# Performance work log

Hardware: AMD Instinct MI355X
Metric: run time of the kernel (lower is better)

The kernel has to match this reference:

```python
import jax, jax.numpy as jnp
import numpy as np

DIM = 1024
NUM_HEADS = 16
HEAD_DIM = DIM // NUM_HEADS
SCALE = HEAD_DIM ** -0.5


def setup_inputs() -> dict:
    key = jax.random.key(0)
    ks = jax.random.split(key, 5)
    x = jax.random.normal(ks[0], (4, 1024, DIM), dtype=jnp.float32)
    w_qkv = jax.random.normal(ks[1], (DIM, 3 * DIM), dtype=jnp.float32) * (DIM ** -0.5)
    b_qkv = jnp.zeros((3 * DIM,), dtype=jnp.float32)
    w_proj = jax.random.normal(ks[2], (DIM, DIM), dtype=jnp.float32) * (DIM ** -0.5)
    b_proj = jnp.zeros((DIM,), dtype=jnp.float32)
    return {"x": x, "w_qkv": w_qkv, "b_qkv": b_qkv, "w_proj": w_proj, "b_proj": b_proj}


def reference(x, w_qkv, b_qkv, w_proj, b_proj):
    B, N, C = x.shape
    qkv = x @ w_qkv + b_qkv                                  # [B, N, 3C]
    qkv = qkv.reshape(B, N, 3, NUM_HEADS, HEAD_DIM)
    qkv = jnp.transpose(qkv, (2, 0, 3, 1, 4))                # [3, B, H, N, d]
    q, k, v = qkv[0] * SCALE, qkv[1], qkv[2]
    # attn scores in float32 (clamp to finfo range is a no-op after the cast)
    attn = jnp.einsum('bhnd,bhmd->bhnm', q, k).astype(jnp.float32)
    f32 = jnp.finfo(jnp.float32)
    attn = jnp.clip(attn, f32.min, f32.max)
    attn = jax.nn.softmax(attn, axis=-1)
    out = jnp.einsum('bhnm,bhmd->bhnd', attn, v)             # [B, H, N, d]
    out = jnp.transpose(out, (0, 2, 1, 3)).reshape(B, N, C)
    return out @ w_proj + b_proj
```

## Files before the change

### kernel.cpp

```cpp
#include <hip/hip_runtime.h>


typedef _Float16 half8 __attribute__((ext_vector_type(8)));
typedef _Float16 half4v __attribute__((ext_vector_type(4)));
typedef __fp16 fp16x2 __attribute__((ext_vector_type(2)));
typedef float floatx4 __attribute__((ext_vector_type(4)));

#define MFMA16(a, b, c) __builtin_amdgcn_mfma_f32_16x16x32_f16((a), (b), (c), 0, 0, 0)

static constexpr int DIM = 1024;
static constexpr int BATCH = 4;
static constexpr int SEQ = 1024;
static constexpr int NH = 16;
static constexpr int HD = 64;
static constexpr float SCALE = 0.125f;

__device__ static inline void gld16(_Float16* lds, const _Float16* g) {
    __builtin_amdgcn_global_load_lds(
        (const __attribute__((address_space(1))) void*)g,
        (__attribute__((address_space(3))) void*)lds, 16, 0, 0);
}

__global__ __launch_bounds__(256) void prep(const float* __restrict__ x,
                                            _Float16* __restrict__ xh,
                                            const float* __restrict__ wqkv,
                                            _Float16* __restrict__ wqkvT,
                                            const float* __restrict__ wproj,
                                            _Float16* __restrict__ wprojT) {
    __shared__ float tile[32][33];
    const int bid = blockIdx.x;
    const int tid = threadIdx.x;
    if (bid < 4096) {
        int i = (bid * 256 + tid) * 4;
        float4 v = *reinterpret_cast<const float4*>(x + i);
        half4v h;
        h[0] = (_Float16)v.x; h[1] = (_Float16)v.y;
        h[2] = (_Float16)v.z; h[3] = (_Float16)v.w;
        const int m = i >> 10, k = i & 1023;
        *reinterpret_cast<half4v*>(
            &xh[((size_t)(k >> 5) * 4096 + m) * 32 + (k & 31)]) = h;
        return;
    }
    const float* in;
    _Float16* out;
    int C, NN, bx, by;
    if (bid < 7168) {
        int b = bid - 4096;
        in = wqkv; out = wqkvT; C = 3072; NN = 3072;
        bx = b % 96; by = b / 96;
    } else {
        int b = bid - 7168;
        in = wproj; out = wprojT; C = 1024; NN = 1024;
        bx = b & 31; by = b >> 5;
    }
    const int c0 = bx * 32, r0 = by * 32;
    const int tx = tid & 31, ty = tid >> 5;
#pragma unroll
    for (int j = 0; j < 32; j += 8)
        tile[ty + j][tx] = in[(size_t)(r0 + ty + j) * C + (c0 + tx)];
    __syncthreads();
#pragma unroll
    for (int j = 0; j < 32; j += 8)
        out[((size_t)(r0 >> 5) * NN + (c0 + ty + j)) * 32 + tx] =
            (_Float16)tile[tx][ty + j];
}

template <int MODE>
__global__ __launch_bounds__(256) void gemm_bt(const _Float16* __restrict__ A,
                                               const _Float16* __restrict__ Bt,
                                               const float* __restrict__ bias, int N,
                                               float* __restrict__ outF,
                                               _Float16* __restrict__ qbuf,
                                               _Float16* __restrict__ kbuf,
                                               _Float16* __restrict__ vtbuf) {
    constexpr int NT = 32;
    __shared__ _Float16 S[4][2][4096];

    const int tid = threadIdx.x;
    const int wid = tid >> 6;
    const int lane = tid & 63;
    const int g = lane >> 4;
    const int ln = lane & 15;
    const int wr = wid >> 1, wc = wid & 1;
    const int m0 = blockIdx.y * 128;
    const int n0 = blockIdx.x * 128;
    const size_t PA = (size_t)4096 * 32;
    const size_t PB = (size_t)N * 32;
    const int lsw = (lane >> 2) * 32 + (((lane & 3) ^ ((lane >> 3) & 3)) * 8);
    const int gsw = (g ^ ((ln >> 1) & 3)) * 8;
    const _Float16* ga = A + ((size_t)(m0 + wr * 64)) * 32 + lsw;
    const _Float16* gb = Bt + ((size_t)(n0 + wc * 64)) * 32 + lsw;
    _Float16* Sw = &S[wid][0][0];

    floatx4 acc[4][4];
#pragma unroll
    for (int i = 0; i < 4; ++i)
#pragma unroll
        for (int j = 0; j < 4; ++j) acc[i][j] = (floatx4){0.f, 0.f, 0.f, 0.f};

#pragma unroll
    for (int c = 0; c < 4; ++c) {
        gld16(Sw + c * 512, ga + c * 512);
        gld16(Sw + 2048 + c * 512, gb + c * 512);
    }

    for (int kt = 0; kt < NT; ++kt) {
        const int cur = kt & 1;
        if (kt < NT - 1) {
            const size_t ka = (size_t)(kt + 1) * PA;
            const size_t kb = (size_t)(kt + 1) * PB;
            _Float16* Sn = Sw + (cur ^ 1) * 4096;
#pragma unroll
            for (int c = 0; c < 4; ++c) {
                gld16(Sn + c * 512, ga + ka + c * 512);
                gld16(Sn + 2048 + c * 512, gb + kb + c * 512);
            }
            asm volatile("s_waitcnt vmcnt(8)" ::: "memory");
        } else {
            asm volatile("s_waitcnt vmcnt(0)" ::: "memory");
        }
        const _Float16* Sc = Sw + cur * 4096;

        half8 af[4], bf[4];
#pragma unroll
        for (int i = 0; i < 4; ++i)
            af[i] = *reinterpret_cast<const half8*>(&Sc[(i * 16 + ln) * 32 + gsw]);
#pragma unroll
        for (int j = 0; j < 4; ++j)
            bf[j] = *reinterpret_cast<const half8*>(&Sc[2048 + (j * 16 + ln) * 32 + gsw]);
#pragma unroll
        for (int i = 0; i < 4; ++i)
#pragma unroll
            for (int j = 0; j < 4; ++j) acc[i][j] = MFMA16(af[i], bf[j], acc[i][j]);
    }

#pragma unroll
    for (int i = 0; i < 4; ++i) {
#pragma unroll
        for (int j = 0; j < 4; ++j) {
            const int n = n0 + wc * 64 + j * 16 + ln;
            const float bn = bias[n];
            const int mrow = m0 + wr * 64 + i * 16 + g * 4;
            if (MODE == 0) {
                const int which = n >> 10;
                const int rem = n & 1023;
                const int h = rem >> 6;
                const int dd = rem & 63;
                const int b = mrow >> 10, tok = mrow & 1023;
                const int bh = b * NH + h;
                if (which == 2) {
                    half4v pk;
#pragma unroll
                    for (int r = 0; r < 4; ++r) pk[r] = (_Float16)(acc[i][j][r] + bn);
                    *reinterpret_cast<half4v*>(
                        &vtbuf[((size_t)(bh * 32 + (tok >> 5)) * 64 + dd) * 32 +
                               (tok & 31)]) = pk;
                } else if (which == 1) {
#pragma unroll
                    for (int r = 0; r < 4; ++r)
                        kbuf[((size_t)(bh * 2 + (dd >> 5)) * SEQ + tok + r) * 32 +
                             (dd & 31)] = (_Float16)(acc[i][j][r] + bn);
                } else {
#pragma unroll
                    for (int r = 0; r < 4; ++r)
                        qbuf[(size_t)((bh << 10) + tok + r) * HD + dd] =
                            (_Float16)((acc[i][j][r] + bn) * SCALE);
                }
            } else {
#pragma unroll
                for (int r = 0; r < 4; ++r)
                    outF[(size_t)(mrow + r) * N + n] = acc[i][j][r] + bn;
            }
        }
    }
}

__global__ __launch_bounds__(256, 4) void flash_attn(const _Float16* __restrict__ qbuf,
                                                     const _Float16* __restrict__ kbuf,
                                                     const _Float16* __restrict__ vtbuf,
                                                     _Float16* __restrict__ attn_out) {
    __shared__ _Float16 Klds[2 * 4096];
    __shared__ _Float16 Vlds[2 * 4096];

    const int tid = threadIdx.x;
    const int wid = tid >> 6;
    const int lane = tid & 63;
    const int g = lane >> 4;
    const int ln = lane & 15;
    const int bh = blockIdx.x;
    const int qbase = blockIdx.y * 64 + wid * 16;
    const _Float16* qg = qbuf + ((size_t)bh << 10) * HD;
    const _Float16* kg = kbuf + (size_t)bh * (2 * SEQ * 32);
    const _Float16* vg = vtbuf + (size_t)bh * (32 * 64 * 32);

    const int woff = wid * 512;
    const int lsw = (lane >> 2) * 32 + (((lane & 3) ^ ((lane >> 3) & 3)) * 8);
    const int gsw = (g ^ ((ln >> 1) & 3)) * 8;
    const int sl0 = ((lane >> 4) & 1) * 32 + ln;
    const bool hi32 = (lane & 32) != 0;

    half8 qf[2];
#pragma unroll
    for (int f = 0; f < 2; ++f)
        qf[f] = *reinterpret_cast<const half8*>(
            qg + (size_t)(qbase + ln) * HD + f * 32 + g * 8);

    floatx4 o[4];
#pragma unroll
    for (int t = 0; t < 4; ++t) o[t] = (floatx4){0.f, 0.f, 0.f, 0.f};
    float l_lane = 0.f;

    constexpr int NT = SEQ / 64;
#pragma unroll
    for (int f = 0; f < 2; ++f) {
        gld16(&Klds[f * 2048 + woff], kg + (size_t)f * (SEQ * 32) + woff + lsw);
        gld16(&Vlds[f * 2048 + woff], vg + (size_t)f * 2048 + woff + lsw);
    }

    for (int kt = 0; kt < NT; ++kt) {
        asm volatile("s_waitcnt vmcnt(0)" ::: "memory");
        asm volatile("s_barrier" ::: "memory");
        const int cur = kt & 1;
        if (kt < NT - 1) {
            const int nb = cur ^ 1;
#pragma unroll
            for (int f = 0; f < 2; ++f) {
                gld16(&Klds[nb * 4096 + f * 2048 + woff],
                      kg + (size_t)f * (SEQ * 32) + (kt + 1) * 2048 + woff + lsw);
                gld16(&Vlds[nb * 4096 + f * 2048 + woff],
                      vg + (size_t)(2 * (kt + 1) + f) * 2048 + woff + lsw);
            }
        }
        const _Float16* Kb = &Klds[cur * 4096];
        const _Float16* Vb = &Vlds[cur * 4096];

        half8 kf[4][2], vf[4][2];
#pragma unroll
        for (int c = 0; c < 4; ++c)
#pragma unroll
            for (int f = 0; f < 2; ++f) {
                kf[c][f] = *reinterpret_cast<const half8*>(
                    &Kb[f * 2048 + (c * 16 + ln) * 32 + gsw]);
                vf[c][f] = *reinterpret_cast<const half8*>(
                    &Vb[f * 2048 + (c * 16 + ln) * 32 + gsw]);
            }

        floatx4 st[4];
#pragma unroll
        for (int c = 0; c < 4; ++c) {
            floatx4 z = (floatx4){0.f, 0.f, 0.f, 0.f};
            z = MFMA16(kf[c][0], qf[0], z);
            z = MFMA16(kf[c][1], qf[1], z);
            st[c] = z;
        }

        int pk[4][2];
#pragma unroll
        for (int c = 0; c < 4; ++c) {
            float p0 = __expf(st[c][0]);
            float p1 = __expf(st[c][1]);
            float p2 = __expf(st[c][2]);
            float p3 = __expf(st[c][3]);
            l_lane += (p0 + p1) + (p2 + p3);
            union { fp16x2 h; int i; } u0, u1;
            u0.h = __builtin_amdgcn_cvt_pkrtz(p0, p1);
            u1.h = __builtin_amdgcn_cvt_pkrtz(p2, p3);
            pk[c][0] = u0.i;
            pk[c][1] = u1.i;
        }

#pragma unroll
        for (int H = 0; H < 2; ++H) {
            int a0 = __shfl(pk[2 * H][0], sl0), b0 = __shfl(pk[2 * H + 1][0], sl0);
            int a1 = __shfl(pk[2 * H][1], sl0), b1 = __shfl(pk[2 * H + 1][1], sl0);
            int a2 = __shfl(pk[2 * H][0], sl0 + 16), b2 = __shfl(pk[2 * H + 1][0], sl0 + 16);
            int a3 = __shfl(pk[2 * H][1], sl0 + 16), b3 = __shfl(pk[2 * H + 1][1], sl0 + 16);
            union { int i[4]; half8 h; } ua;
            ua.i[0] = hi32 ? b0 : a0;
            ua.i[1] = hi32 ? b1 : a1;
            ua.i[2] = hi32 ? b2 : a2;
            ua.i[3] = hi32 ? b3 : a3;
#pragma unroll
            for (int t = 0; t < 4; ++t) o[t] = MFMA16(ua.h, vf[t][H], o[t]);
        }
    }

    l_lane += __shfl_xor(l_lane, 16);
    l_lane += __shfl_xor(l_lane, 32);

    const int b = bh >> 4, h = bh & 15;
#pragma unroll
    for (int r = 0; r < 4; ++r) {
        const float inv = 1.0f / __shfl(l_lane, g * 4 + r);
        const int tok = qbase + g * 4 + r;
#pragma unroll
        for (int t = 0; t < 4; ++t)
            attn_out[((size_t)(h * 2 + (t >> 1)) * 4096 + (b * SEQ + tok)) * 32 +
                     (t & 1) * 16 + ln] = (_Float16)(o[t][r] * inv);
    }
}

extern "C" void kernel_launch(void* const* d_in, const int* in_sizes, int n_in,
                              void* d_out, int out_size, void* d_ws, size_t ws_size,
                              hipStream_t stream) {
    const float* x = (const float*)d_in[0];
    const float* wqkv = (const float*)d_in[1];
    const float* bqkv = (const float*)d_in[2];
    const float* wproj = (const float*)d_in[3];
    const float* bproj = (const float*)d_in[4];
    float* out = (float*)d_out;

    char* ws = (char*)d_ws;
    _Float16* xh     = (_Float16*)(ws);
    _Float16* wqkvT  = (_Float16*)(ws + (8ull << 20));
    _Float16* qbuf   = (_Float16*)(ws + (14ull << 20));
    _Float16* kbuf   = (_Float16*)(ws + (22ull << 20));
    _Float16* vtbuf  = (_Float16*)(ws + (30ull << 20));
    _Float16* wprojT = (_Float16*)(ws + (38ull << 20));
    _Float16* attn   = xh;

    prep<<<8192, 256, 0, stream>>>(x, xh, wqkv, wqkvT, wproj, wprojT);
    gemm_bt<0><<<dim3(24, 32), 256, 0, stream>>>(xh, wqkvT, bqkv, 3 * DIM, nullptr,
                                                 qbuf, kbuf, vtbuf);
    flash_attn<<<dim3(BATCH * NH, SEQ / 64), 256, 0, stream>>>(qbuf, kbuf, vtbuf, attn);
    gemm_bt<1><<<dim3(8, 32), 256, 0, stream>>>(attn, wprojT, bproj, DIM, out,
                                                nullptr, nullptr, nullptr);
}
```

Measured before the change: 177.3 us.

## Use 256x256-tile 512-thread GEMM with 4-stage LDS pipeline for QKV projection

Adds a new gemm256 kernel with 256x256 output tiles, 8 waves, and a 4-buffer global_load_lds pipeline that issues next-stage loads interleaved with MFMA halves, and uses it for the QKV projection instead of the 128x128 gemm_bt. Larger tiles raise arithmetic intensity and cut global/L2 traffic per FLOP, and the deeper prefetch hides load latency. The grid shrinks to 192 blocks, fewer than the number of CUs on the device, so per-CU occupancy and load balance may suffer. Register pressure from 32 accumulators per wave is also a risk.

```diff
diff --git a/kernel.cpp b/kernel.cpp
--- a/kernel.cpp
+++ b/kernel.cpp
@@ -66,6 +66,135 @@
 }
 
 template <int MODE>
+__global__ __launch_bounds__(512, 2) void gemm256(const _Float16* __restrict__ A,
+                                                  const _Float16* __restrict__ Bt,
+                                                  const float* __restrict__ bias,
+                                                  int N, float* __restrict__ outF,
+                                                  _Float16* __restrict__ qbuf,
+                                                  _Float16* __restrict__ kbuf,
+                                                  _Float16* __restrict__ vtbuf) {
+    __shared__ __align__(16) _Float16 S[4][16384];
+
+    const int tid = threadIdx.x;
+    const int wid = tid >> 6;
+    const int lane = tid & 63;
+    const int g = lane >> 4;
+    const int ln = lane & 15;
+    const int wr = wid >> 2, wc = wid & 3;
+    const int m0 = blockIdx.y * 256;
+    const int n0 = blockIdx.x * 256;
+    const size_t PA = (size_t)4096 * 32;
+    const size_t PB = (size_t)N * 32;
+    const int lsw = (lane >> 2) * 32 + (((lane & 3) ^ ((lane >> 3) & 3)) * 8);
+    const int gsw = (g ^ ((ln >> 1) & 3)) * 8;
+    const _Float16* ga = A + ((size_t)(m0 + wid * 32)) * 32 + lsw;
+    const _Float16* gb = Bt + ((size_t)(n0 + wid * 32)) * 32 + lsw;
+
+    floatx4 acc[8][4];
+#pragma unroll
+    for (int i = 0; i < 8; ++i)
+#pragma unroll
+        for (int j = 0; j < 4; ++j) acc[i][j] = (floatx4){0.f, 0.f, 0.f, 0.f};
+
+#define STAGE_A(t)                                                      \
+    do {                                                                \
+        const _Float16* s_ = ga + (size_t)(t) * PA;                     \
+        _Float16* d_ = &S[(t) & 3][wid * 1024];                         \
+        gld16(d_, s_);                                                  \
+        gld16(d_ + 512, s_ + 512);                                      \
+    } while (0)
+#define STAGE_B(t)                                                      \
+    do {                                                                \
+        const _Float16* s_ = gb + (size_t)(t) * PB;                     \
+        _Float16* d_ = &S[(t) & 3][8192 + wid * 1024];                  \
+        gld16(d_, s_);                                                  \
+        gld16(d_ + 512, s_ + 512);                                      \
+    } while (0)
+
+    STAGE_A(0); STAGE_B(0);
+    STAGE_A(1); STAGE_B(1);
+    STAGE_A(2); STAGE_B(2);
+
+#define COMPUTE_HALF(Sc, rh)                                                     \
+    do {                                                                         \
+        half8 af[4];                                                             \
+        _Pragma("unroll") for (int i = 0; i < 4; ++i) af[i] =                    \
+            *reinterpret_cast<const half8*>(                                     \
+                &(Sc)[(wr * 128 + (rh) * 64 + i * 16 + ln) * 32 + gsw]);         \
+        __builtin_amdgcn_s_setprio(1);                                           \
+        _Pragma("unroll") for (int i = 0; i < 4; ++i)                            \
+            _Pragma("unroll") for (int j = 0; j < 4; ++j) acc[(rh) * 4 + i][j] = \
+                MFMA16(af[i], bf[j], acc[(rh) * 4 + i][j]);                      \
+        __builtin_amdgcn_s_setprio(0);                                           \
+    } while (0)
+
+#define GEMM_STEP(t, DO_STAGE, GATE_N)                                          \
+    do {                                                                        \
+        asm volatile("s_waitcnt vmcnt(" GATE_N ")" ::: "memory");               \
+        __builtin_amdgcn_s_barrier();                                           \
+        const _Float16* Sc = &S[(t) & 3][0];                                    \
+        if (DO_STAGE) STAGE_A((t) + 3);                                         \
+        half8 bf[4];                                                            \
+        _Pragma("unroll") for (int j = 0; j < 4; ++j) bf[j] =                   \
+            *reinterpret_cast<const half8*>(                                    \
+                &Sc[8192 + (wc * 64 + j * 16 + ln) * 32 + gsw]);                \
+        COMPUTE_HALF(Sc, 0);                                                    \
+        if (DO_STAGE) STAGE_B((t) + 3);                                        \
+        COMPUTE_HALF(Sc, 1);                                                    \
+    } while (0)
+
+    for (int t = 0; t < 29; ++t) GEMM_STEP(t, true, "8");
+    GEMM_STEP(29, false, "8");
+    GEMM_STEP(30, false, "4");
+    GEMM_STEP(31, false, "0");
+
+#undef GEMM_STEP
+#undef COMPUTE_HALF
+#undef STAGE_A
+#undef STAGE_B
+
+#pragma unroll
+    for (int i = 0; i < 8; ++i) {
+#pragma unroll
+        for (int j = 0; j < 4; ++j) {
+            const int n = n0 + wc * 64 + j * 16 + ln;
+            const float bn = bias[n];
+            const int mrow = m0 + wr * 128 + i * 16 + g * 4;
+            if (MODE == 0) {
+                const int which = n >> 10;
+                const int rem = n & 1023;
+                const int h = rem >> 6;
+                const int dd = rem & 63;
+                const int b = mrow >> 10, tok = mrow & 1023;
+                const int bh = b * NH + h;
+                if (which == 2) {
+                    half4v pk;
+#pragma unroll
+                    for (int r = 0; r < 4; ++r) pk[r] = (_Float16)(acc[i][j][r] + bn);
+                    *reinterpret_cast<half4v*>(
+                        &vtbuf[((size_t)(bh * 32 + (tok >> 5)) * 64 + dd) * 32 +
+                               (tok & 31)]) = pk;
+                } else if (which == 1) {
+#pragma unroll
+                    for (int r = 0; r < 4; ++r)
+                        kbuf[((size_t)(bh * 2 + (dd >> 5)) * SEQ + tok + r) * 32 +
+                             (dd & 31)] = (_Float16)(acc[i][j][r] + bn);
+                } else {
+#pragma unroll
+                    for (int r = 0; r < 4; ++r)
+                        qbuf[(size_t)((bh << 10) + tok + r) * HD + dd] =
+                            (_Float16)((acc[i][j][r] + bn) * SCALE);
+                }
+            } else {
+#pragma unroll
+                for (int r = 0; r < 4; ++r)
+                    outF[(size_t)(mrow + r) * N + n] = acc[i][j][r] + bn;
+            }
+        }
+    }
+}
+
+template <int MODE>
 __global__ __launch_bounds__(256) void gemm_bt(const _Float16* __restrict__ A,
                                                const _Float16* __restrict__ Bt,
                                                const float* __restrict__ bias, int N,
@@ -320,7 +449,7 @@
     _Float16* attn   = xh;
 
     prep<<<8192, 256, 0, stream>>>(x, xh, wqkv, wqkvT, wproj, wprojT);
-    gemm_bt<0><<<dim3(24, 32), 256, 0, stream>>>(xh, wqkvT, bqkv, 3 * DIM, nullptr,
+    gemm256<0><<<dim3(12, 16), 512, 0, stream>>>(xh, wqkvT, bqkv, 3 * DIM, nullptr,
                                                  qbuf, kbuf, vtbuf);
     flash_attn<<<dim3(BATCH * NH, SEQ / 64), 256, 0, stream>>>(qbuf, kbuf, vtbuf, attn);
     gemm_bt<1><<<dim3(8, 32), 256, 0, stream>>>(attn, wprojT, bproj, DIM, out,
```

Result: faster. 170.4 us (-3.9%).

## Rewrite GEMMs with shared LDS tiles, 4-stage pipeline and larger QKV tiles

Applied to the files above, without the earlier changes.

Replaces the templated per-wave GEMM, where each wave loaded its own private A/B tiles, with two specialised kernels of 512 threads. All eight waves now share one block-wide LDS tile, and a 4-deep global_load_lds ring uses barriers, staggered waitcnts and s_setprio around the MFMA bursts. The QKV GEMM moves to 256x192 tiles (a 16x16 grid) to raise data reuse per block. The change aims to cut redundant global/LDS traffic and hide load latency. In exchange it adds barrier synchronisation, uses more LDS per block, and launches fewer blocks, which may underfill the CUs.

```diff
diff --git a/kernel.cpp b/kernel.cpp
--- a/kernel.cpp
+++ b/kernel.cpp
@@ -65,16 +65,134 @@
             (_Float16)tile[tx][ty + j];
 }
 
-template <int MODE>
-__global__ __launch_bounds__(256) void gemm_bt(const _Float16* __restrict__ A,
-                                               const _Float16* __restrict__ Bt,
-                                               const float* __restrict__ bias, int N,
-                                               float* __restrict__ outF,
-                                               _Float16* __restrict__ qbuf,
-                                               _Float16* __restrict__ kbuf,
-                                               _Float16* __restrict__ vtbuf) {
-    constexpr int NT = 32;
-    __shared__ _Float16 S[4][2][4096];
+__global__ __launch_bounds__(512, 2) void gemm_qkv(const _Float16* __restrict__ A,
+                                                   const _Float16* __restrict__ Bt,
+                                                   const float* __restrict__ bias,
+                                                   _Float16* __restrict__ qbuf,
+                                                   _Float16* __restrict__ kbuf,
+                                                   _Float16* __restrict__ vtbuf) {
+    __shared__ __align__(16) _Float16 S[4][14336];
+
+    const int tid = threadIdx.x;
+    const int wid = tid >> 6;
+    const int lane = tid & 63;
+    const int g = lane >> 4;
+    const int ln = lane & 15;
+    const int wr = wid >> 1, wc = wid & 1;
+    const int m0 = blockIdx.y * 256;
+    const int n0 = blockIdx.x * 192;
+    const bool wlt4 = wid < 4;
+    const size_t PA = (size_t)4096 * 32;
+    const size_t PB = (size_t)3072 * 32;
+    const int lsw = (lane >> 2) * 32 + (((lane & 3) ^ ((lane >> 3) & 3)) * 8);
+    const int gsw = (g ^ ((ln >> 1) & 3)) * 8;
+    const _Float16* ga0 = A + (size_t)(m0 + wid * 16) * 32 + lsw;
+    const _Float16* ga1 = A + (size_t)(m0 + (wid + 8) * 16) * 32 + lsw;
+    const _Float16* gb0 = Bt + (size_t)(n0 + wid * 16) * 32 + lsw;
+    const _Float16* gb1 = Bt + (size_t)(n0 + (wid + 8) * 16) * 32 + lsw;
+
+    floatx4 acc[4][6];
+#pragma unroll
+    for (int i = 0; i < 4; ++i)
+#pragma unroll
+        for (int j = 0; j < 6; ++j) acc[i][j] = (floatx4){0.f, 0.f, 0.f, 0.f};
+
+#define STAGE_A(t)                                                      \
+    do {                                                                \
+        gld16(&S[(t) & 3][wid * 512], ga0 + (size_t)(t) * PA);          \
+        gld16(&S[(t) & 3][(wid + 8) * 512], ga1 + (size_t)(t) * PA);    \
+    } while (0)
+#define STAGE_B(t)                                                      \
+    do {                                                                \
+        gld16(&S[(t) & 3][8192 + wid * 512], gb0 + (size_t)(t) * PB);   \
+        if (wlt4)                                                       \
+            gld16(&S[(t) & 3][8192 + (wid + 8) * 512],                  \
+                  gb1 + (size_t)(t) * PB);                              \
+    } while (0)
+
+    STAGE_A(0); STAGE_B(0);
+    STAGE_A(1); STAGE_B(1);
+    STAGE_A(2); STAGE_B(2);
+
+#define COMPUTE_HALF(Sc, hh)                                                   \
+    do {                                                                       \
+        half8 af[2];                                                           \
+        _Pragma("unroll") for (int i = 0; i < 2; ++i) af[i] =                  \
+            *reinterpret_cast<const half8*>(                                   \
+                &(Sc)[(wr * 64 + (hh) * 32 + i * 16 + ln) * 32 + gsw]);        \
+        __builtin_amdgcn_s_setprio(1);                                         \
+        _Pragma("unroll") for (int i = 0; i < 2; ++i)                          \
+            _Pragma("unroll") for (int j = 0; j < 6; ++j)                      \
+                acc[(hh) * 2 + i][j] = MFMA16(af[i], bf[j], acc[(hh) * 2 + i][j]); \
+        __builtin_amdgcn_s_setprio(0);                                         \
+    } while (0)
+
+#define QKV_STEP(t, DO_STAGE, G4, G3)                                          \
+    do {                                                                       \
+        if (wlt4) asm volatile("s_waitcnt vmcnt(" G4 ")" ::: "memory");        \
+        else      asm volatile("s_waitcnt vmcnt(" G3 ")" ::: "memory");        \
+        __builtin_amdgcn_s_barrier();                                          \
+        const _Float16* Sc = &S[(t) & 3][0];                                   \
+        if (DO_STAGE) STAGE_A((t) + 3);                                        \
+        half8 bf[6];                                                           \
+        _Pragma("unroll") for (int j = 0; j < 6; ++j) bf[j] =                  \
+            *reinterpret_cast<const half8*>(                                   \
+                &Sc[8192 + (wc * 96 + j * 16 + ln) * 32 + gsw]);               \
+        COMPUTE_HALF(Sc, 0);                                                   \
+        if (DO_STAGE) STAGE_B((t) + 3);                                        \
+        COMPUTE_HALF(Sc, 1);                                                   \
+    } while (0)
+
+    for (int t = 0; t < 29; ++t) QKV_STEP(t, true, "8", "6");
+    QKV_STEP(29, false, "8", "6");
+    QKV_STEP(30, false, "4", "3");
+    QKV_STEP(31, false, "0", "0");
+
+#undef QKV_STEP
+#undef COMPUTE_HALF
+#undef STAGE_A
+#undef STAGE_B
+
+#pragma unroll
+    for (int i = 0; i < 4; ++i) {
+#pragma unroll
+        for (int j = 0; j < 6; ++j) {
+            const int n = n0 + wc * 96 + j * 16 + ln;
+            const float bn = bias[n];
+            const int mrow = m0 + wr * 64 + i * 16 + g * 4;
+            const int which = n >> 10;
+            const int rem = n & 1023;
+            const int h = rem >> 6;
+            const int dd = rem & 63;
+            const int b = mrow >> 10, tok = mrow & 1023;
+            const int bh = b * NH + h;
+            if (which == 2) {
+                half4v pk;
+#pragma unroll
+                for (int r = 0; r < 4; ++r) pk[r] = (_Float16)(acc[i][j][r] + bn);
+                *reinterpret_cast<half4v*>(
+                    &vtbuf[((size_t)(bh * 32 + (tok >> 5)) * 64 + dd) * 32 +
+                           (tok & 31)]) = pk;
+            } else if (which == 1) {
+#pragma unroll
+                for (int r = 0; r < 4; ++r)
+                    kbuf[((size_t)(bh * 2 + (dd >> 5)) * SEQ + tok + r) * 32 +
+                         (dd & 31)] = (_Float16)(acc[i][j][r] + bn);
+            } else {
+#pragma unroll
+                for (int r = 0; r < 4; ++r)
+                    qbuf[(size_t)((bh << 10) + tok + r) * HD + dd] =
+                        (_Float16)((acc[i][j][r] + bn) * SCALE);
+            }
+        }
+    }
+}
+
+__global__ __launch_bounds__(512, 2) void gemm_proj(const _Float16* __restrict__ A,
+                                                    const _Float16* __restrict__ Bt,
+                                                    const float* __restrict__ bias,
+                                                    float* __restrict__ outF) {
+    __shared__ __align__(16) _Float16 S[4][8192];
 
     const int tid = threadIdx.x;
     const int wid = tid >> 6;
@@ -85,92 +203,70 @@
     const int m0 = blockIdx.y * 128;
     const int n0 = blockIdx.x * 128;
     const size_t PA = (size_t)4096 * 32;
-    const size_t PB = (size_t)N * 32;
+    const size_t PB = (size_t)1024 * 32;
     const int lsw = (lane >> 2) * 32 + (((lane & 3) ^ ((lane >> 3) & 3)) * 8);
     const int gsw = (g ^ ((ln >> 1) & 3)) * 8;
-    const _Float16* ga = A + ((size_t)(m0 + wr * 64)) * 32 + lsw;
-    const _Float16* gb = Bt + ((size_t)(n0 + wc * 64)) * 32 + lsw;
-    _Float16* Sw = &S[wid][0][0];
-
-    floatx4 acc[4][4];
-#pragma unroll
-    for (int i = 0; i < 4; ++i)
+    const _Float16* ga = A + (size_t)(m0 + wid * 16) * 32 + lsw;
+    const _Float16* gb = Bt + (size_t)(n0 + wid * 16) * 32 + lsw;
+
+    floatx4 acc[2][4];
+#pragma unroll
+    for (int i = 0; i < 2; ++i)
 #pragma unroll
         for (int j = 0; j < 4; ++j) acc[i][j] = (floatx4){0.f, 0.f, 0.f, 0.f};
 
-#pragma unroll
-    for (int c = 0; c < 4; ++c) {
-        gld16(Sw + c * 512, ga + c * 512);
-        gld16(Sw + 2048 + c * 512, gb + c * 512);
-    }
-
-    for (int kt = 0; kt < NT; ++kt) {
-        const int cur = kt & 1;
-        if (kt < NT - 1) {
-            const size_t ka = (size_t)(kt + 1) * PA;
-            const size_t kb = (size_t)(kt + 1) * PB;
-            _Float16* Sn = Sw + (cur ^ 1) * 4096;
-#pragma unroll
-            for (int c = 0; c < 4; ++c) {
-                gld16(Sn + c * 512, ga + ka + c * 512);
-                gld16(Sn + 2048 + c * 512, gb + kb + c * 512);
-            }
-            asm volatile("s_waitcnt vmcnt(8)" ::: "memory");
-        } else {
-            asm volatile("s_waitcnt vmcnt(0)" ::: "memory");
-        }
-        const _Float16* Sc = Sw + cur * 4096;
-
-        half8 af[4], bf[4];
-#pragma unroll
-        for (int i = 0; i < 4; ++i)
-            af[i] = *reinterpret_cast<const half8*>(&Sc[(i * 16 + ln) * 32 + gsw]);
-#pragma unroll
-        for (int j = 0; j < 4; ++j)
-            bf[j] = *reinterpret_cast<const half8*>(&Sc[2048 + (j * 16 + ln) * 32 + gsw]);
-#pragma unroll
-        for (int i = 0; i < 4; ++i)
-#pragma unroll
-            for (int j = 0; j < 4; ++j) acc[i][j] = MFMA16(af[i], bf[j], acc[i][j]);
-    }
-
-#pragma unroll
-    for (int i = 0; i < 4; ++i) {
+#define STAGE_A(t) gld16(&S[(t) & 3][wid * 512], ga + (size_t)(t) * PA)
+#define STAGE_B(t) gld16(&S[(t) & 3][4096 + wid * 512], gb + (size_t)(t) * PB)
+
+    STAGE_A(0); STAGE_B(0);
+    STAGE_A(1); STAGE_B(1);
+    STAGE_A(2); STAGE_B(2);
+
+#define COMPUTE_HALF(Sc, hh)                                                   \
+    do {                                                                       \
+        half8 af = *reinterpret_cast<const half8*>(                            \
+            &(Sc)[(wr * 32 + (hh) * 16 + ln) * 32 + gsw]);                     \
+        __builtin_amdgcn_s_setprio(1);                                         \
+        _Pragma("unroll") for (int j = 0; j < 4; ++j)                          \
+            acc[hh][j] = MFMA16(af, bf[j], acc[hh][j]);                        \
+        __builtin_amdgcn_s_setprio(0);                                         \
+    } while (0)
+
+#define PROJ_STEP(t, DO_STAGE, GN)                                             \
+    do {                                                                       \
+        asm volatile("s_waitcnt vmcnt(" GN ")" ::: "memory");                  \
+        __builtin_amdgcn_s_barrier();                                          \
+        const _Float16* Sc = &S[(t) & 3][0];                                   \
+        if (DO_STAGE) STAGE_A((t) + 3);                                        \
+        half8 bf[4];                                                           \
+        _Pragma("unroll") for (int j = 0; j < 4; ++j) bf[j] =                  \
+            *reinterpret_cast<const half8*>(                                   \
+                &Sc[4096 + (wc * 64 + j * 16 + ln) * 32 + gsw]);               \
+        COMPUTE_HALF(Sc, 0);                                                   \
+        if (DO_STAGE) STAGE_B((t) + 3);                                        \
+        COMPUTE_HALF(Sc, 1);                                                   \
+    } while (0)
+
+    for (int t = 0; t < 29; ++t) PROJ_STEP(t, true, "4");
+    PROJ_STEP(29, false, "4");
+    PROJ_STEP(30, false, "2");
+    PROJ_STEP(31, false, "0");
+
+#undef PROJ_STEP
+#undef COMPUTE_HALF
+#undef STAGE_A
+#undef STAGE_B
+
+#pragma unroll
+    for (int i = 0; i < 2; ++i) {
 #pragma unroll
         for (int j = 0; j < 4; ++j) {
             const int n = n0 + wc * 64 + j * 16 + ln;
             const float bn = bias[n];
-            const int mrow = m0 + wr * 64 + i * 16 + g * 4;
-            if (MODE == 0) {
-                const int which = n >> 10;
-                const int rem = n & 1023;
-                const int h = rem >> 6;
-                const int dd = rem & 63;
-                const int b = mrow >> 10, tok = mrow & 1023;
-                const int bh = b * NH + h;
-                if (which == 2) {
-                    half4v pk;
-#pragma unroll
-                    for (int r = 0; r < 4; ++r) pk[r] = (_Float16)(acc[i][j][r] + bn);
-                    *reinterpret_cast<half4v*>(
-                        &vtbuf[((size_t)(bh * 32 + (tok >> 5)) * 64 + dd) * 32 +
-                               (tok & 31)]) = pk;
-                } else if (which == 1) {
-#pragma unroll
-                    for (int r = 0; r < 4; ++r)
-                        kbuf[((size_t)(bh * 2 + (dd >> 5)) * SEQ + tok + r) * 32 +
-                             (dd & 31)] = (_Float16)(acc[i][j][r] + bn);
-                } else {
-#pragma unroll
-                    for (int r = 0; r < 4; ++r)
-                        qbuf[(size_t)((bh << 10) + tok + r) * HD + dd] =
-                            (_Float16)((acc[i][j][r] + bn) * SCALE);
-                }
-            } else {
-#pragma unroll
-                for (int r = 0; r < 4; ++r)
-                    outF[(size_t)(mrow + r) * N + n] = acc[i][j][r] + bn;
-            }
+            const int mrow = m0 + wr * 32 + i * 16 + g * 4;
+#pragma unroll
+            for (int r = 0; r < 4; ++r)
+                outF[(size_t)(mrow + r) * 1024 + n] = acc[i][j][r] + bn;
         }
     }
 }
@@ -320,9 +416,7 @@
     _Float16* attn   = xh;
 
     prep<<<8192, 256, 0, stream>>>(x, xh, wqkv, wqkvT, wproj, wprojT);
-    gemm_bt<0><<<dim3(24, 32), 256, 0, stream>>>(xh, wqkvT, bqkv, 3 * DIM, nullptr,
-                                                 qbuf, kbuf, vtbuf);
+    gemm_qkv<<<dim3(16, 16), 512, 0, stream>>>(xh, wqkvT, bqkv, qbuf, kbuf, vtbuf);
     flash_attn<<<dim3(BATCH * NH, SEQ / 64), 256, 0, stream>>>(qbuf, kbuf, vtbuf, attn);
-    gemm_bt<1><<<dim3(8, 32), 256, 0, stream>>>(attn, wprojT, bproj, DIM, out,
-                                                nullptr, nullptr, nullptr);
-}
+    gemm_proj<<<dim3(8, 32), 512, 0, stream>>>(attn, wprojT, bproj, out);
+}
```

Result: faster. 163.1 us (-8.0%).
